# Kernel tuning notes

Measured on AMD Instinct MI355X. Metric: run time of the kernel, lower is better.

The kernel has to match this reference:

```python
import jax, jax.numpy as jnp
import numpy as np

BALANCE_FACTOR = 10.0  # from init_kwargs


def _foreground_mask(bboxes, H, W):
    # bboxes: [B, N, 4] int (x1, y1, x2, y2), half-open raster [y1:y2, x1:x2].
    # 2D difference-array (summed-area) trick: scatter +/-1 at box corners,
    # then double cumsum; count > 0 <=> pixel covered by >= 1 box.
    B, N, _ = bboxes.shape
    x1 = jnp.clip(bboxes[..., 0], 0, W)
    y1 = jnp.clip(bboxes[..., 1], 0, H)
    x2 = jnp.clip(bboxes[..., 2], 0, W)
    y2 = jnp.clip(bboxes[..., 3], 0, H)
    b = jnp.broadcast_to(jnp.arange(B)[:, None], (B, N))
    one = jnp.ones((B, N), jnp.int32)
    diff = jnp.zeros((B, H + 1, W + 1), jnp.int32)
    diff = (diff.at[b, y1, x1].add(one)
                .at[b, y1, x2].add(-one)
                .at[b, y2, x1].add(-one)
                .at[b, y2, x2].add(one))
    cnt = jnp.cumsum(jnp.cumsum(diff, axis=1), axis=2)[:, :H, :W]
    return cnt > 0  # [B, H, W] bool


def setup_inputs() -> dict:
    key = jax.random.key(0)
    k1, k2, k3 = jax.random.split(key, 3)
    B, H, W, N = 8, 1024, 1024, 64
    loss = jax.random.uniform(k1, (B, H, W), dtype=jnp.float32)
    pred_densities = jax.random.uniform(k2, (B, H, W), dtype=jnp.float32)
    # random valid boxes: sort coordinate pairs so x1<=x2, y1<=y2
    raw = jax.random.randint(k3, (B, N, 2, 2), 0, 1024)  # [...,(x pair),(y pair)]
    xs = jnp.sort(raw[..., 0, :], axis=-1)  # [B,N,2]
    ys = jnp.sort(raw[..., 1, :], axis=-1)  # [B,N,2]
    bboxes = jnp.stack([xs[..., 0], ys[..., 0], xs[..., 1], ys[..., 1]], axis=-1).astype(jnp.int32)
    return {"loss": loss, "pred_densities": pred_densities, "bboxes": bboxes}


def reference(loss, pred_densities, bboxes):
    B, H, W = pred_densities.shape[:3]
    fg = _foreground_mask(bboxes, H, W)  # [B,H,W] bool
    # weights = fg * balance_factor + background
    weights = jnp.where(fg, jnp.float32(BALANCE_FACTOR), jnp.float32(1.0))
    out = loss * weights
    # normalize_loss with mask=None: divide by n_pixels (H*W) then by n_img (B)
    out = out / jnp.float32(H * W)
    out = out / jnp.float32(B)
    return out
```

## Files before the change

### kernel.cpp

```cpp
#include <hip/hip_runtime.h>


#define NBOX 64
#define WIDTH 1024

__global__ __launch_bounds__(256) void density_loss_row_kernel(
    const float* __restrict__ loss,
    const int*   __restrict__ bboxes,
    float*       __restrict__ out)
{
    __shared__ int4 sbox[NBOX];
    __shared__ unsigned int part[256];

    const int t   = threadIdx.x;
    const int row = blockIdx.x;
    const int b   = row >> 10;
    const int y   = row & 1023;

    if (t < NBOX)
        sbox[t] = reinterpret_cast<const int4*>(bboxes)[b * NBOX + t];
    __syncthreads();

    {
        const int word = t >> 3;
        const int g    = t & 7;
        const int lo_w = word << 5;
        unsigned int m = 0u;
        #pragma unroll
        for (int j = 0; j < 8; ++j) {
            const int4 bx = sbox[g * 8 + j];
            const bool yin = (y >= bx.y) && (y < bx.w);
            const int lo = max(bx.x, lo_w);
            const int hi = min(bx.z, lo_w + 32);
            if (yin && (lo < hi)) {
                const int len = hi - lo;
                const unsigned int mask =
                    (len >= 32) ? 0xFFFFFFFFu : ((1u << len) - 1u);
                m |= mask << (lo - lo_w);
            }
        }
        part[t] = m;
    }
    __syncthreads();

    const int wbase = (t >> 3) << 3;
    const unsigned int cov =
        part[wbase + 0] | part[wbase + 1] | part[wbase + 2] | part[wbase + 3] |
        part[wbase + 4] | part[wbase + 5] | part[wbase + 6] | part[wbase + 7];

    const size_t base = (size_t)row * WIDTH;
    const float4 l = reinterpret_cast<const float4*>(loss + base)[t];
    const int sh = (t & 7) << 2;
    const float C = 0x1p-23f;

    float4 o;
    o.x = (l.x * (((cov >> (sh + 0)) & 1u) ? 10.0f : 1.0f)) * C;
    o.y = (l.y * (((cov >> (sh + 1)) & 1u) ? 10.0f : 1.0f)) * C;
    o.z = (l.z * (((cov >> (sh + 2)) & 1u) ? 10.0f : 1.0f)) * C;
    o.w = (l.w * (((cov >> (sh + 3)) & 1u) ? 10.0f : 1.0f)) * C;
    reinterpret_cast<float4*>(out + base)[t] = o;
}

extern "C" void kernel_launch(void* const* d_in, const int* in_sizes, int n_in,
                              void* d_out, int out_size, void* d_ws, size_t ws_size,
                              hipStream_t stream) {
    const float* loss   = (const float*)d_in[0];
    const int*   bboxes = (const int*)d_in[2];
    float*       out    = (float*)d_out;

    const int n_rows = 8 * 1024;
    density_loss_row_kernel<<<dim3(n_rows), dim3(256), 0, stream>>>(loss, bboxes, out);
}
```

Before: 106.8 us.

## Compute per-thread box coverage directly, dropping shared-memory staging and block syncs

Each thread now loops over all 64 boxes read straight from global memory (uniform, cacheable loads) and builds a 4-bit coverage mask for its own four pixels. This removes the shared-memory box staging, the partial-word reduction through shared memory, and both __syncthreads barriers. In exchange each thread does eight times as many box tests (64 instead of 8) with uniform-branch scalar loads, adding ALU and scalar-load work to a kernel that is otherwise memory-bound.

```diff
diff --git a/kernel.cpp b/kernel.cpp
--- a/kernel.cpp
+++ b/kernel.cpp
@@ -2,62 +2,40 @@
 
 
 #define NBOX 64
-#define WIDTH 1024
 
-__global__ __launch_bounds__(256) void density_loss_row_kernel(
+__global__ __launch_bounds__(256) void density_loss_kernel(
     const float* __restrict__ loss,
-    const int*   __restrict__ bboxes,
+    const int4*  __restrict__ bboxes,
     float*       __restrict__ out)
 {
-    __shared__ int4 sbox[NBOX];
-    __shared__ unsigned int part[256];
-
-    const int t   = threadIdx.x;
     const int row = blockIdx.x;
     const int b   = row >> 10;
     const int y   = row & 1023;
+    const int t   = threadIdx.x;
+    const int px0 = t << 2;
 
-    if (t < NBOX)
-        sbox[t] = reinterpret_cast<const int4*>(bboxes)[b * NBOX + t];
-    __syncthreads();
+    const int4* __restrict__ box = bboxes + b * NBOX;
 
-    {
-        const int word = t >> 3;
-        const int g    = t & 7;
-        const int lo_w = word << 5;
-        unsigned int m = 0u;
-        #pragma unroll
-        for (int j = 0; j < 8; ++j) {
-            const int4 bx = sbox[g * 8 + j];
-            const bool yin = (y >= bx.y) && (y < bx.w);
-            const int lo = max(bx.x, lo_w);
-            const int hi = min(bx.z, lo_w + 32);
-            if (yin && (lo < hi)) {
-                const int len = hi - lo;
-                const unsigned int mask =
-                    (len >= 32) ? 0xFFFFFFFFu : ((1u << len) - 1u);
-                m |= mask << (lo - lo_w);
-            }
+    unsigned int m = 0u;
+    for (int i = 0; i < NBOX; ++i) {
+        const int4 bx = box[i];
+        if (y >= bx.y && y < bx.w) {
+            const int lo = max(bx.x, px0);
+            const int hi = min(bx.z, px0 + 4);
+            if (lo < hi)
+                m |= ((1u << (hi - lo)) - 1u) << (lo - px0);
         }
-        part[t] = m;
     }
-    __syncthreads();
 
-    const int wbase = (t >> 3) << 3;
-    const unsigned int cov =
-        part[wbase + 0] | part[wbase + 1] | part[wbase + 2] | part[wbase + 3] |
-        part[wbase + 4] | part[wbase + 5] | part[wbase + 6] | part[wbase + 7];
-
-    const size_t base = (size_t)row * WIDTH;
+    const size_t base = (size_t)row << 10;
     const float4 l = reinterpret_cast<const float4*>(loss + base)[t];
-    const int sh = (t & 7) << 2;
     const float C = 0x1p-23f;
 
     float4 o;
-    o.x = (l.x * (((cov >> (sh + 0)) & 1u) ? 10.0f : 1.0f)) * C;
-    o.y = (l.y * (((cov >> (sh + 1)) & 1u) ? 10.0f : 1.0f)) * C;
-    o.z = (l.z * (((cov >> (sh + 2)) & 1u) ? 10.0f : 1.0f)) * C;
-    o.w = (l.w * (((cov >> (sh + 3)) & 1u) ? 10.0f : 1.0f)) * C;
+    o.x = (l.x * ((m & 1u) ? 10.0f : 1.0f)) * C;
+    o.y = (l.y * ((m & 2u) ? 10.0f : 1.0f)) * C;
+    o.z = (l.z * ((m & 4u) ? 10.0f : 1.0f)) * C;
+    o.w = (l.w * ((m & 8u) ? 10.0f : 1.0f)) * C;
     reinterpret_cast<float4*>(out + base)[t] = o;
 }
 
@@ -65,9 +43,9 @@
                               void* d_out, int out_size, void* d_ws, size_t ws_size,
                               hipStream_t stream) {
     const float* loss   = (const float*)d_in[0];
-    const int*   bboxes = (const int*)d_in[2];
+    const int4*  bboxes = (const int4*)d_in[2];
     float*       out    = (float*)d_out;
 
     const int n_rows = 8 * 1024;
-    density_loss_row_kernel<<<dim3(n_rows), dim3(256), 0, stream>>>(loss, bboxes, out);
+    density_loss_kernel<<<dim3(n_rows), dim3(256), 0, stream>>>(loss, bboxes, out);
 }
```

Result: slower. 120.9 us (+13.2%).
